# Kernel optimization log

Measured on AMD Instinct MI355X. Metric: run time of the kernel, lower is better.

Reference implementation:

```python
import jax, jax.numpy as jnp
import numpy as np

B, T, V, E, DH, H, M, W = 64, 50, 32000, 64, 128, 8, 256, 50


def setup_inputs() -> dict:
    key = jax.random.key(0)
    ks = jax.random.split(key, 18)
    sc = 0.02
    return {
        "x": jax.random.randint(ks[0], (B, T), 0, V),
        "tok_emb": jax.random.normal(ks[1], (V, E)) * sc,
        "pos_emb": jax.random.normal(ks[2], (W, E)) * sc,
        "Wq": jax.random.normal(ks[3], (H, E, DH)) * sc,
        "bq": jnp.zeros((H, DH)),
        "Wk": jax.random.normal(ks[4], (H, E, DH)) * sc,
        "bk": jnp.zeros((H, DH)),
        "Wv": jax.random.normal(ks[5], (H, E, DH)) * sc,
        "bv": jnp.zeros((H, DH)),
        "Wo": jax.random.normal(ks[6], (H * DH, E)) * sc,
        "bo": jnp.zeros((E,)),
        "W1": jax.random.normal(ks[7], (E, M)) * sc,
        "b1": jnp.zeros((M,)),
        "W2": jax.random.normal(ks[8], (M, E)) * sc,
        "b2": jnp.zeros((E,)),
        "Wf": jax.random.normal(ks[9], (E, V)) * sc,
        "bf": jnp.zeros((V,)),
    }


def reference(x, tok_emb, pos_emb, Wq, bq, Wk, bk, Wv, bv, Wo, bo, W1, b1, W2, b2, Wf, bf):
    b, t = x.shape
    h = tok_emb[x] + pos_emb[:t]  # [B,T,E]
    # batched per-head QKV projections (original loops over 8 heads)
    Q = jnp.einsum("bte,hed->bhtd", h, Wq) + bq[None, :, None, :]
    K = jnp.einsum("bte,hed->bhtd", h, Wk) + bk[None, :, None, :]
    Vv = jnp.einsum("bte,hed->bhtd", h, Wv) + bv[None, :, None, :]
    scores = jnp.einsum("bhtd,bhsd->bhts", Q, K) / (DH ** 0.5)
    # faithful to original: masked_fill(tril(scores) == 0, -inf)
    scores = jnp.where(jnp.tril(scores) == 0, -jnp.inf, scores)
    attn = jax.nn.softmax(scores, axis=-1)
    o = jnp.einsum("bhts,bhsd->bhtd", attn, Vv)
    o = o.transpose(0, 2, 1, 3).reshape(b, t, H * DH)  # concat heads
    a = o @ Wo + bo
    # NOTE: no residual connections in the original module
    m = jax.nn.gelu(a @ W1 + b1, approximate=False)
    y = m @ W2 + b2
    logits = y @ Wf + bf  # [B,T,V]
    return logits
```

## Files before the change

### kernel.cpp

```cpp
#include <hip/hip_runtime.h>
#include <math.h>

#define T_ 50
#define R_ 3200

using u16 = unsigned short;
typedef __attribute__((ext_vector_type(8))) __bf16 bf16x8;
typedef __attribute__((ext_vector_type(4))) float f32x4;

__device__ __forceinline__ float bf2f(u16 u) {
  union { unsigned int i; float f; } x; x.i = ((unsigned int)u) << 16; return x.f;
}
__device__ __forceinline__ u16 f2bf(float f) {
  union { float f; unsigned int i; } x; x.f = f;
  unsigned int r = x.i + 0x7FFFu + ((x.i >> 16) & 1u);
  return (u16)(r >> 16);
}
__device__ __forceinline__ void split2(float v, u16& hi, u16& lo) {
  hi = f2bf(v);
  lo = f2bf(v - bf2f(hi));
}
__device__ __forceinline__ float gelu_f(float v) {
  return 0.5f * v * (1.0f + erff(v * 0.70710678118654752f));
}

__global__ __launch_bounds__(256) void k_embed(const int* __restrict__ x,
    const float* __restrict__ tok, const float* __restrict__ pos,
    float* __restrict__ h) {
  int i = blockIdx.x * 256 + threadIdx.x;
  if (i >= R_ * 64) return;
  int row = i >> 6, e = i & 63;
  int t = row % T_;
  int v = x[row];
  h[i] = tok[(long)v * 64 + e] + pos[t * 64 + e];
}

__global__ __launch_bounds__(256) void k_pack(
    const float* __restrict__ Wq, const float* __restrict__ Wk, const float* __restrict__ Wv,
    const float* __restrict__ bq, const float* __restrict__ bk, const float* __restrict__ bv,
    const float* __restrict__ Wo, const float* __restrict__ W1, const float* __restrict__ W2,
    u16* __restrict__ WqkvTh, u16* __restrict__ WqkvTl, float* __restrict__ bqkv,
    u16* __restrict__ WoTh, u16* __restrict__ WoTl,
    u16* __restrict__ W1Th, u16* __restrict__ W1Tl,
    u16* __restrict__ W2Th, u16* __restrict__ W2Tl) {
  int i = blockIdx.x * 256 + threadIdx.x;
  const int S0 = 196608, S1 = 3072, S2 = 65536, S3 = 16384;
  if (i < S0) {
    int n = i >> 6, e = i & 63;
    int p = n >> 10, rem = n & 1023;
    int hh = rem >> 7, d = rem & 127;
    const float* W = (p == 0) ? Wq : ((p == 1) ? Wk : Wv);
    split2(W[hh * 8192 + e * 128 + d], WqkvTh[i], WqkvTl[i]);
    return;
  }
  i -= S0;
  if (i < S1) { int p = i >> 10, rem = i & 1023;
    const float* bb = (p == 0) ? bq : ((p == 1) ? bk : bv);
    bqkv[i] = bb[rem]; return; }
  i -= S1;
  if (i < S2) { int n = i >> 10, k = i & 1023;
    split2(Wo[k * 64 + n], WoTh[i], WoTl[i]); return; }
  i -= S2;
  if (i < S3) { int n = i >> 6, k = i & 63;
    split2(W1[k * 256 + n], W1Th[i], W1Tl[i]); return; }
  i -= S3;
  { int n = i >> 8, k = i & 255;
    split2(W2[k * 64 + n], W2Th[i], W2Tl[i]); }
}

__global__ __launch_bounds__(256) void k_transpose_wf(const float* __restrict__ Wf,
    u16* __restrict__ WfTh, u16* __restrict__ WfTl) {
  __shared__ __align__(16) float tile[64][68];
  int n0 = blockIdx.x * 64;
  for (int c = threadIdx.x; c < 1024; c += 256) {
    int k = c >> 4, ch = (c & 15) * 4;
    *(float4*)&tile[k][ch] = *(const float4*)&Wf[(long)k * 32000 + n0 + ch];
  }
  __syncthreads();
  for (int c = threadIdx.x; c < 1024; c += 256) {
    int n = c >> 4, ch = (c & 15) * 4;
    u16 th[4], tl[4];
#pragma unroll
    for (int j = 0; j < 4; ++j) split2(tile[ch + j][n], th[j], tl[j]);
    *(ushort4*)&WfTh[(long)(n0 + n) * 64 + ch] = *(ushort4*)th;
    *(ushort4*)&WfTl[(long)(n0 + n) * 64 + ch] = *(ushort4*)tl;
  }
}

__global__ __launch_bounds__(256) void k_attn(const float* __restrict__ QKV,
                                              float* __restrict__ O) {
  int bh = blockIdx.x;
  int b = bh >> 3, hd = bh & 7;
  __shared__ __align__(16) float Kl[T_][128];
  __shared__ __align__(16) float Vl[T_][128];
  const int tid = threadIdx.x, lane = tid & 63, wave = tid >> 6;
  const float* base = QKV + (long)b * T_ * 3072 + hd * 128;
  for (int c = tid; c < T_ * 32; c += 256) {
    int s = c >> 5, c4 = (c & 31) * 4;
    *(float4*)&Kl[s][c4] = *(const float4*)&base[(long)s * 3072 + 1024 + c4];
    *(float4*)&Vl[s][c4] = *(const float4*)&base[(long)s * 3072 + 2048 + c4];
  }
  __syncthreads();
  const float scale = 0.0883883476483184406f;
  for (int r = wave; r < T_; r += 4) {
    float q0 = base[(long)r * 3072 + lane];
    float q1 = base[(long)r * 3072 + 64 + lane];
    float sc = -INFINITY;
    for (int s = 0; s <= r; ++s) {
      float p = q0 * Kl[s][lane] + q1 * Kl[s][64 + lane];
      p += __shfl_xor(p, 32); p += __shfl_xor(p, 16); p += __shfl_xor(p, 8);
      p += __shfl_xor(p, 4);  p += __shfl_xor(p, 2);  p += __shfl_xor(p, 1);
      if (lane == s) sc = p * scale;
    }
    float mx = sc;
    mx = fmaxf(mx, __shfl_xor(mx, 32)); mx = fmaxf(mx, __shfl_xor(mx, 16));
    mx = fmaxf(mx, __shfl_xor(mx, 8));  mx = fmaxf(mx, __shfl_xor(mx, 4));
    mx = fmaxf(mx, __shfl_xor(mx, 2));  mx = fmaxf(mx, __shfl_xor(mx, 1));
    float e = expf(sc - mx);
    float sum = e;
    sum += __shfl_xor(sum, 32); sum += __shfl_xor(sum, 16); sum += __shfl_xor(sum, 8);
    sum += __shfl_xor(sum, 4);  sum += __shfl_xor(sum, 2);  sum += __shfl_xor(sum, 1);
    float pr = e / sum;
    float o0 = 0.f, o1 = 0.f;
    for (int s = 0; s <= r; ++s) {
      float p = __shfl(pr, s);
      o0 += p * Vl[s][lane];
      o1 += p * Vl[s][64 + lane];
    }
    long orow = ((long)b * T_ + r) * 1024 + hd * 128;
    O[orow + lane] = o0;
    O[orow + 64 + lane] = o1;
  }
}

template <int BN, int ACT>
__global__ __launch_bounds__(256) void k_gemm(
    const float* __restrict__ A, int lda,
    const u16* __restrict__ Bth, const u16* __restrict__ Btl,
    const float* __restrict__ bias, float* __restrict__ C, int ldc, int K) {
  constexpr int BM = 64, BK = 64;
  constexpr int TN = BN / 16;
  __shared__ __align__(16) u16 Ah[BM][BK + 8];
  __shared__ __align__(16) u16 Al[BM][BK + 8];
  __shared__ __align__(16) u16 Bh[BN][BK + 8];
  __shared__ __align__(16) u16 Bl[BN][BK + 8];
  const int m0 = blockIdx.x * BM;
  const int n0 = blockIdx.y * BN;
  const int tid = threadIdx.x;
  const int lane = tid & 63, wave = tid >> 6;
  const int ln = lane & 15, quad = lane >> 4;
  const int wm = wave * 16;
  f32x4 acc[TN];
#pragma unroll
  for (int tn = 0; tn < TN; ++tn)
#pragma unroll
    for (int i = 0; i < 4; ++i) acc[tn][i] = 0.f;

  for (int kk = 0; kk < K; kk += BK) {
    for (int c = tid; c < BM * 16; c += 256) {
      int r = c >> 4, c4 = (c & 15) * 4;
      float4 v = *(const float4*)&A[(long)(m0 + r) * lda + kk + c4];
      u16 th[4], tl[4];
      split2(v.x, th[0], tl[0]); split2(v.y, th[1], tl[1]);
      split2(v.z, th[2], tl[2]); split2(v.w, th[3], tl[3]);
      *(ushort4*)&Ah[r][c4] = *(ushort4*)th;
      *(ushort4*)&Al[r][c4] = *(ushort4*)tl;
    }
    for (int c = tid; c < BN * 8; c += 256) {
      int r = c >> 3, c8 = (c & 7) * 8;
      *(uint4*)&Bh[r][c8] = *(const uint4*)&Bth[(long)(n0 + r) * K + kk + c8];
      *(uint4*)&Bl[r][c8] = *(const uint4*)&Btl[(long)(n0 + r) * K + kk + c8];
    }
    __syncthreads();
#pragma unroll
    for (int ks = 0; ks < BK / 32; ++ks) {
      bf16x8 ah = *(const bf16x8*)&Ah[wm + ln][ks * 32 + quad * 8];
      bf16x8 al = *(const bf16x8*)&Al[wm + ln][ks * 32 + quad * 8];
#pragma unroll
      for (int tn = 0; tn < TN; ++tn) {
        bf16x8 bh = *(const bf16x8*)&Bh[tn * 16 + ln][ks * 32 + quad * 8];
        bf16x8 bl = *(const bf16x8*)&Bl[tn * 16 + ln][ks * 32 + quad * 8];
        acc[tn] = __builtin_amdgcn_mfma_f32_16x16x32_bf16(ah, bh, acc[tn], 0, 0, 0);
        acc[tn] = __builtin_amdgcn_mfma_f32_16x16x32_bf16(al, bh, acc[tn], 0, 0, 0);
        acc[tn] = __builtin_amdgcn_mfma_f32_16x16x32_bf16(ah, bl, acc[tn], 0, 0, 0);
      }
    }
    __syncthreads();
  }
#pragma unroll
  for (int tn = 0; tn < TN; ++tn) {
    int col = n0 + tn * 16 + ln;
    float bv = bias[col];
#pragma unroll
    for (int r = 0; r < 4; ++r) {
      float v = acc[tn][r] + bv;
      if (ACT) v = gelu_f(v);
      C[(long)(m0 + wm + quad * 4 + r) * ldc + col] = v;
    }
  }
}

extern "C" void kernel_launch(void* const* d_in, const int* in_sizes, int n_in,
                              void* d_out, int out_size, void* d_ws, size_t ws_size,
                              hipStream_t stream) {
  const int*   x   = (const int*)d_in[0];
  const float* tok = (const float*)d_in[1];
  const float* pos = (const float*)d_in[2];
  const float* Wq  = (const float*)d_in[3];
  const float* bq  = (const float*)d_in[4];
  const float* Wk  = (const float*)d_in[5];
  const float* bk  = (const float*)d_in[6];
  const float* Wv  = (const float*)d_in[7];
  const float* bv  = (const float*)d_in[8];
  const float* Wo  = (const float*)d_in[9];
  const float* bo  = (const float*)d_in[10];
  const float* W1  = (const float*)d_in[11];
  const float* b1  = (const float*)d_in[12];
  const float* W2  = (const float*)d_in[13];
  const float* b2  = (const float*)d_in[14];
  const float* Wf  = (const float*)d_in[15];
  const float* bfv = (const float*)d_in[16];

  char* ws = (char*)d_ws;
  float* h      = (float*)(ws + 0);
  float* QKV    = (float*)(ws + 819200);
  float* o      = (float*)(ws + 40140800);
  float* a      = (float*)(ws + 53248000);
  float* m      = (float*)(ws + 54067200);
  float* y      = (float*)(ws + 57344000);
  u16*  WqkvTh  = (u16*)(ws + 58163200);
  u16*  WqkvTl  = (u16*)(ws + 58556416);
  float* bqkv   = (float*)(ws + 58949632);
  u16*  WoTh    = (u16*)(ws + 58961920);
  u16*  WoTl    = (u16*)(ws + 59092992);
  u16*  W1Th    = (u16*)(ws + 59224064);
  u16*  W1Tl    = (u16*)(ws + 59256832);
  u16*  W2Th    = (u16*)(ws + 59289600);
  u16*  W2Tl    = (u16*)(ws + 59322368);
  u16*  WfTh    = (u16*)(ws + 59355136);
  u16*  WfTl    = (u16*)(ws + 63451136);
  float* out    = (float*)d_out;

  k_embed<<<dim3(800), 256, 0, stream>>>(x, tok, pos, h);
  k_pack<<<dim3(1164), 256, 0, stream>>>(Wq, Wk, Wv, bq, bk, bv, Wo, W1, W2,
      WqkvTh, WqkvTl, bqkv, WoTh, WoTl, W1Th, W1Tl, W2Th, W2Tl);
  k_transpose_wf<<<dim3(500), 256, 0, stream>>>(Wf, WfTh, WfTl);
  k_gemm<128, 0><<<dim3(50, 24), 256, 0, stream>>>(h, 64, WqkvTh, WqkvTl, bqkv, QKV, 3072, 64);
  k_attn<<<dim3(512), 256, 0, stream>>>(QKV, o);
  k_gemm<64, 0><<<dim3(50, 1), 256, 0, stream>>>(o, 1024, WoTh, WoTl, bo, a, 64, 1024);
  k_gemm<128, 1><<<dim3(50, 2), 256, 0, stream>>>(a, 64, W1Th, W1Tl, b1, m, 256, 64);
  k_gemm<64, 0><<<dim3(50, 1), 256, 0, stream>>>(m, 256, W2Th, W2Tl, b2, y, 64, 256);
  k_gemm<128, 0><<<dim3(50, 250), 256, 0, stream>>>(y, 64, WfTh, WfTl, bfv, out, 32000, 64);
}
```

Measured before the change: 736.6 us.

## Fuse prep kernels, pre-split activations to bf16 hi/lo, restructure attention

Merges the embed, weight-pack and Wf-transpose kernels into one launch. Producers now emit activations already split into bf16 hi/lo pairs, so the GEMMs read their A operands straight from global memory instead of converting through shared memory. The Wo and W2 GEMMs use a larger K tile. Attention switches from per-key wave reductions to one key per lane through a padded K tile in LDS. This cuts launches and per-tile conversion work, at the cost of uncoalesced direct A-fragment loads and extra LDS traffic.

```diff
diff --git a/kernel.cpp b/kernel.cpp
--- a/kernel.cpp
+++ b/kernel.cpp
@@ -24,54 +24,55 @@
   return 0.5f * v * (1.0f + erff(v * 0.70710678118654752f));
 }
 
-__global__ __launch_bounds__(256) void k_embed(const int* __restrict__ x,
-    const float* __restrict__ tok, const float* __restrict__ pos,
-    float* __restrict__ h) {
-  int i = blockIdx.x * 256 + threadIdx.x;
-  if (i >= R_ * 64) return;
-  int row = i >> 6, e = i & 63;
-  int t = row % T_;
-  int v = x[row];
-  h[i] = tok[(long)v * 64 + e] + pos[t * 64 + e];
-}
-
-__global__ __launch_bounds__(256) void k_pack(
+__global__ __launch_bounds__(256) void k_prep(
+    const int* __restrict__ x, const float* __restrict__ tok, const float* __restrict__ pos,
     const float* __restrict__ Wq, const float* __restrict__ Wk, const float* __restrict__ Wv,
     const float* __restrict__ bq, const float* __restrict__ bk, const float* __restrict__ bv,
     const float* __restrict__ Wo, const float* __restrict__ W1, const float* __restrict__ W2,
+    const float* __restrict__ Wf,
+    u16* __restrict__ hH, u16* __restrict__ hL,
     u16* __restrict__ WqkvTh, u16* __restrict__ WqkvTl, float* __restrict__ bqkv,
     u16* __restrict__ WoTh, u16* __restrict__ WoTl,
     u16* __restrict__ W1Th, u16* __restrict__ W1Tl,
-    u16* __restrict__ W2Th, u16* __restrict__ W2Tl) {
-  int i = blockIdx.x * 256 + threadIdx.x;
-  const int S0 = 196608, S1 = 3072, S2 = 65536, S3 = 16384;
-  if (i < S0) {
-    int n = i >> 6, e = i & 63;
-    int p = n >> 10, rem = n & 1023;
-    int hh = rem >> 7, d = rem & 127;
-    const float* W = (p == 0) ? Wq : ((p == 1) ? Wk : Wv);
-    split2(W[hh * 8192 + e * 128 + d], WqkvTh[i], WqkvTl[i]);
-    return;
-  }
-  i -= S0;
-  if (i < S1) { int p = i >> 10, rem = i & 1023;
-    const float* bb = (p == 0) ? bq : ((p == 1) ? bk : bv);
-    bqkv[i] = bb[rem]; return; }
-  i -= S1;
-  if (i < S2) { int n = i >> 10, k = i & 1023;
-    split2(Wo[k * 64 + n], WoTh[i], WoTl[i]); return; }
-  i -= S2;
-  if (i < S3) { int n = i >> 6, k = i & 63;
-    split2(W1[k * 256 + n], W1Th[i], W1Tl[i]); return; }
-  i -= S3;
-  { int n = i >> 8, k = i & 255;
-    split2(W2[k * 64 + n], W2Th[i], W2Tl[i]); }
-}
-
-__global__ __launch_bounds__(256) void k_transpose_wf(const float* __restrict__ Wf,
+    u16* __restrict__ W2Th, u16* __restrict__ W2Tl,
     u16* __restrict__ WfTh, u16* __restrict__ WfTl) {
   __shared__ __align__(16) float tile[64][68];
-  int n0 = blockIdx.x * 64;
+  int bid = blockIdx.x;
+  if (bid < 800) {
+    int i = bid * 256 + threadIdx.x;
+    int row = i >> 6, e = i & 63;
+    int t = row % T_;
+    int v = x[row];
+    split2(tok[(long)v * 64 + e] + pos[t * 64 + e], hH[i], hL[i]);
+    return;
+  }
+  if (bid < 1964) {
+    int i = (bid - 800) * 256 + threadIdx.x;
+    const int S0 = 196608, S1 = 3072, S2 = 65536, S3 = 16384;
+    if (i < S0) {
+      int n = i >> 6, e = i & 63;
+      int p = n >> 10, rem = n & 1023;
+      int hh_ = rem >> 7, d = rem & 127;
+      const float* W = (p == 0) ? Wq : ((p == 1) ? Wk : Wv);
+      split2(W[hh_ * 8192 + e * 128 + d], WqkvTh[i], WqkvTl[i]);
+      return;
+    }
+    i -= S0;
+    if (i < S1) { int p = i >> 10, rem = i & 1023;
+      const float* bb = (p == 0) ? bq : ((p == 1) ? bk : bv);
+      bqkv[i] = bb[rem]; return; }
+    i -= S1;
+    if (i < S2) { int n = i >> 10, k = i & 1023;
+      split2(Wo[k * 64 + n], WoTh[i], WoTl[i]); return; }
+    i -= S2;
+    if (i < S3) { int n = i >> 6, k = i & 63;
+      split2(W1[k * 256 + n], W1Th[i], W1Tl[i]); return; }
+    i -= S3;
+    { int n = i >> 8, k = i & 255;
+      split2(W2[k * 64 + n], W2Th[i], W2Tl[i]); }
+    return;
+  }
+  int n0 = (bid - 1964) * 64;
   for (int c = threadIdx.x; c < 1024; c += 256) {
     int k = c >> 4, ch = (c & 15) * 4;
     *(float4*)&tile[k][ch] = *(const float4*)&Wf[(long)k * 32000 + n0 + ch];
@@ -88,30 +89,35 @@
 }
 
 __global__ __launch_bounds__(256) void k_attn(const float* __restrict__ QKV,
-                                              float* __restrict__ O) {
+                                              u16* __restrict__ Oh,
+                                              u16* __restrict__ Ol) {
   int bh = blockIdx.x;
   int b = bh >> 3, hd = bh & 7;
-  __shared__ __align__(16) float Kl[T_][128];
+  __shared__ __align__(16) float Kl[64][133];
   __shared__ __align__(16) float Vl[T_][128];
+  __shared__ float Qw[4][128];
+  __shared__ float Pw[4][64];
   const int tid = threadIdx.x, lane = tid & 63, wave = tid >> 6;
   const float* base = QKV + (long)b * T_ * 3072 + hd * 128;
   for (int c = tid; c < T_ * 32; c += 256) {
     int s = c >> 5, c4 = (c & 31) * 4;
-    *(float4*)&Kl[s][c4] = *(const float4*)&base[(long)s * 3072 + 1024 + c4];
+    float4 kv = *(const float4*)&base[(long)s * 3072 + 1024 + c4];
+    Kl[s][c4] = kv.x; Kl[s][c4 + 1] = kv.y; Kl[s][c4 + 2] = kv.z; Kl[s][c4 + 3] = kv.w;
     *(float4*)&Vl[s][c4] = *(const float4*)&base[(long)s * 3072 + 2048 + c4];
+  }
+  for (int c = tid; c < 14 * 32; c += 256) {
+    int s = 50 + (c >> 5), c4 = (c & 31) * 4;
+    Kl[s][c4] = 0.f; Kl[s][c4 + 1] = 0.f; Kl[s][c4 + 2] = 0.f; Kl[s][c4 + 3] = 0.f;
   }
   __syncthreads();
   const float scale = 0.0883883476483184406f;
   for (int r = wave; r < T_; r += 4) {
-    float q0 = base[(long)r * 3072 + lane];
-    float q1 = base[(long)r * 3072 + 64 + lane];
-    float sc = -INFINITY;
-    for (int s = 0; s <= r; ++s) {
-      float p = q0 * Kl[s][lane] + q1 * Kl[s][64 + lane];
-      p += __shfl_xor(p, 32); p += __shfl_xor(p, 16); p += __shfl_xor(p, 8);
-      p += __shfl_xor(p, 4);  p += __shfl_xor(p, 2);  p += __shfl_xor(p, 1);
-      if (lane == s) sc = p * scale;
-    }
+    Qw[wave][lane] = base[(long)r * 3072 + lane];
+    Qw[wave][64 + lane] = base[(long)r * 3072 + 64 + lane];
+    float p = 0.f;
+#pragma unroll 8
+    for (int d = 0; d < 128; ++d) p += Qw[wave][d] * Kl[lane][d];
+    float sc = (lane <= r) ? p * scale : -INFINITY;
     float mx = sc;
     mx = fmaxf(mx, __shfl_xor(mx, 32)); mx = fmaxf(mx, __shfl_xor(mx, 16));
     mx = fmaxf(mx, __shfl_xor(mx, 8));  mx = fmaxf(mx, __shfl_xor(mx, 4));
@@ -120,36 +126,37 @@
     float sum = e;
     sum += __shfl_xor(sum, 32); sum += __shfl_xor(sum, 16); sum += __shfl_xor(sum, 8);
     sum += __shfl_xor(sum, 4);  sum += __shfl_xor(sum, 2);  sum += __shfl_xor(sum, 1);
-    float pr = e / sum;
+    Pw[wave][lane] = e / sum;
     float o0 = 0.f, o1 = 0.f;
+#pragma unroll 4
     for (int s = 0; s <= r; ++s) {
-      float p = __shfl(pr, s);
-      o0 += p * Vl[s][lane];
-      o1 += p * Vl[s][64 + lane];
+      float pv = Pw[wave][s];
+      o0 += pv * Vl[s][lane];
+      o1 += pv * Vl[s][64 + lane];
     }
     long orow = ((long)b * T_ + r) * 1024 + hd * 128;
-    O[orow + lane] = o0;
-    O[orow + 64 + lane] = o1;
-  }
-}
-
-template <int BN, int ACT>
+    u16 hi, lo;
+    split2(o0, hi, lo); Oh[orow + lane] = hi;      Ol[orow + lane] = lo;
+    split2(o1, hi, lo); Oh[orow + 64 + lane] = hi; Ol[orow + 64 + lane] = lo;
+  }
+}
+
+template <int BN, int BK, int ACT, int OSPLIT>
 __global__ __launch_bounds__(256) void k_gemm(
-    const float* __restrict__ A, int lda,
+    const u16* __restrict__ Ah, const u16* __restrict__ Al,
     const u16* __restrict__ Bth, const u16* __restrict__ Btl,
-    const float* __restrict__ bias, float* __restrict__ C, int ldc, int K) {
-  constexpr int BM = 64, BK = 64;
+    const float* __restrict__ bias,
+    float* __restrict__ C, u16* __restrict__ Ch, u16* __restrict__ Cl,
+    int ldc, int K) {
+  constexpr int BM = 64;
   constexpr int TN = BN / 16;
-  __shared__ __align__(16) u16 Ah[BM][BK + 8];
-  __shared__ __align__(16) u16 Al[BM][BK + 8];
+  constexpr int BKW = BK / 8;
   __shared__ __align__(16) u16 Bh[BN][BK + 8];
   __shared__ __align__(16) u16 Bl[BN][BK + 8];
-  const int m0 = blockIdx.x * BM;
-  const int n0 = blockIdx.y * BN;
-  const int tid = threadIdx.x;
-  const int lane = tid & 63, wave = tid >> 6;
+  const int m0 = blockIdx.x * BM, n0 = blockIdx.y * BN;
+  const int tid = threadIdx.x, lane = tid & 63, wave = tid >> 6;
   const int ln = lane & 15, quad = lane >> 4;
-  const int wm = wave * 16;
+  const long arow = (long)(m0 + wave * 16 + ln) * K;
   f32x4 acc[TN];
 #pragma unroll
   for (int tn = 0; tn < TN; ++tn)
@@ -157,32 +164,25 @@
     for (int i = 0; i < 4; ++i) acc[tn][i] = 0.f;
 
   for (int kk = 0; kk < K; kk += BK) {
-    for (int c = tid; c < BM * 16; c += 256) {
-      int r = c >> 4, c4 = (c & 15) * 4;
-      float4 v = *(const float4*)&A[(long)(m0 + r) * lda + kk + c4];
-      u16 th[4], tl[4];
-      split2(v.x, th[0], tl[0]); split2(v.y, th[1], tl[1]);
-      split2(v.z, th[2], tl[2]); split2(v.w, th[3], tl[3]);
-      *(ushort4*)&Ah[r][c4] = *(ushort4*)th;
-      *(ushort4*)&Al[r][c4] = *(ushort4*)tl;
-    }
-    for (int c = tid; c < BN * 8; c += 256) {
-      int r = c >> 3, c8 = (c & 7) * 8;
+#pragma unroll
+    for (int c0 = 0; c0 < BN * BKW; c0 += 256) {
+      int c = c0 + tid;
+      int r = c / BKW, c8 = (c % BKW) * 8;
       *(uint4*)&Bh[r][c8] = *(const uint4*)&Bth[(long)(n0 + r) * K + kk + c8];
       *(uint4*)&Bl[r][c8] = *(const uint4*)&Btl[(long)(n0 + r) * K + kk + c8];
     }
     __syncthreads();
 #pragma unroll
     for (int ks = 0; ks < BK / 32; ++ks) {
-      bf16x8 ah = *(const bf16x8*)&Ah[wm + ln][ks * 32 + quad * 8];
-      bf16x8 al = *(const bf16x8*)&Al[wm + ln][ks * 32 + quad * 8];
+      bf16x8 a_h = *(const bf16x8*)&Ah[arow + kk + ks * 32 + quad * 8];
+      bf16x8 a_l = *(const bf16x8*)&Al[arow + kk + ks * 32 + quad * 8];
 #pragma unroll
       for (int tn = 0; tn < TN; ++tn) {
-        bf16x8 bh = *(const bf16x8*)&Bh[tn * 16 + ln][ks * 32 + quad * 8];
-        bf16x8 bl = *(const bf16x8*)&Bl[tn * 16 + ln][ks * 32 + quad * 8];
-        acc[tn] = __builtin_amdgcn_mfma_f32_16x16x32_bf16(ah, bh, acc[tn], 0, 0, 0);
-        acc[tn] = __builtin_amdgcn_mfma_f32_16x16x32_bf16(al, bh, acc[tn], 0, 0, 0);
-        acc[tn] = __builtin_amdgcn_mfma_f32_16x16x32_bf16(ah, bl, acc[tn], 0, 0, 0);
+        bf16x8 b_h = *(const bf16x8*)&Bh[tn * 16 + ln][ks * 32 + quad * 8];
+        bf16x8 b_l = *(const bf16x8*)&Bl[tn * 16 + ln][ks * 32 + quad * 8];
+        acc[tn] = __builtin_amdgcn_mfma_f32_16x16x32_bf16(a_h, b_h, acc[tn], 0, 0, 0);
+        acc[tn] = __builtin_amdgcn_mfma_f32_16x16x32_bf16(a_l, b_h, acc[tn], 0, 0, 0);
+        acc[tn] = __builtin_amdgcn_mfma_f32_16x16x32_bf16(a_h, b_l, acc[tn], 0, 0, 0);
       }
     }
     __syncthreads();
@@ -192,10 +192,16 @@
     int col = n0 + tn * 16 + ln;
     float bv = bias[col];
 #pragma unroll
-    for (int r = 0; r < 4; ++r) {
-      float v = acc[tn][r] + bv;
+    for (int rr = 0; rr < 4; ++rr) {
+      float v = acc[tn][rr] + bv;
       if (ACT) v = gelu_f(v);
-      C[(long)(m0 + wm + quad * 4 + r) * ldc + col] = v;
+      long idx = (long)(m0 + wave * 16 + quad * 4 + rr) * ldc + col;
+      if constexpr (OSPLIT) {
+        u16 hi, lo; split2(v, hi, lo);
+        Ch[idx] = hi; Cl[idx] = lo;
+      } else {
+        C[idx] = v;
+      }
     }
   }
 }
@@ -222,33 +228,42 @@
   const float* bfv = (const float*)d_in[16];
 
   char* ws = (char*)d_ws;
-  float* h      = (float*)(ws + 0);
+  u16*   hH     = (u16*)(ws + 0);
+  u16*   hL     = (u16*)(ws + 409600);
   float* QKV    = (float*)(ws + 819200);
-  float* o      = (float*)(ws + 40140800);
-  float* a      = (float*)(ws + 53248000);
-  float* m      = (float*)(ws + 54067200);
-  float* y      = (float*)(ws + 57344000);
-  u16*  WqkvTh  = (u16*)(ws + 58163200);
-  u16*  WqkvTl  = (u16*)(ws + 58556416);
+  u16*   oH     = (u16*)(ws + 40140800);
+  u16*   oL     = (u16*)(ws + 46694400);
+  u16*   aH     = (u16*)(ws + 53248000);
+  u16*   aL     = (u16*)(ws + 53657600);
+  u16*   mH     = (u16*)(ws + 54067200);
+  u16*   mL     = (u16*)(ws + 55705600);
+  u16*   yH     = (u16*)(ws + 57344000);
+  u16*   yL     = (u16*)(ws + 57753600);
+  u16*   WqkvTh = (u16*)(ws + 58163200);
+  u16*   WqkvTl = (u16*)(ws + 58556416);
   float* bqkv   = (float*)(ws + 58949632);
-  u16*  WoTh    = (u16*)(ws + 58961920);
-  u16*  WoTl    = (u16*)(ws + 59092992);
-  u16*  W1Th    = (u16*)(ws + 59224064);
-  u16*  W1Tl    = (u16*)(ws + 59256832);
-  u16*  W2Th    = (u16*)(ws + 59289600);
-  u16*  W2Tl    = (u16*)(ws + 59322368);
-  u16*  WfTh    = (u16*)(ws + 59355136);
-  u16*  WfTl    = (u16*)(ws + 63451136);
+  u16*   WoTh   = (u16*)(ws + 58961920);
+  u16*   WoTl   = (u16*)(ws + 59092992);
+  u16*   W1Th   = (u16*)(ws + 59224064);
+  u16*   W1Tl   = (u16*)(ws + 59256832);
+  u16*   W2Th   = (u16*)(ws + 59289600);
+  u16*   W2Tl   = (u16*)(ws + 59322368);
+  u16*   WfTh   = (u16*)(ws + 59355136);
+  u16*   WfTl   = (u16*)(ws + 63451136);
   float* out    = (float*)d_out;
 
-  k_embed<<<dim3(800), 256, 0, stream>>>(x, tok, pos, h);
-  k_pack<<<dim3(1164), 256, 0, stream>>>(Wq, Wk, Wv, bq, bk, bv, Wo, W1, W2,
-      WqkvTh, WqkvTl, bqkv, WoTh, WoTl, W1Th, W1Tl, W2Th, W2Tl);
-  k_transpose_wf<<<dim3(500), 256, 0, stream>>>(Wf, WfTh, WfTl);
-  k_gemm<128, 0><<<dim3(50, 24), 256, 0, stream>>>(h, 64, WqkvTh, WqkvTl, bqkv, QKV, 3072, 64);
-  k_attn<<<dim3(512), 256, 0, stream>>>(QKV, o);
-  k_gemm<64, 0><<<dim3(50, 1), 256, 0, stream>>>(o, 1024, WoTh, WoTl, bo, a, 64, 1024);
-  k_gemm<128, 1><<<dim3(50, 2), 256, 0, stream>>>(a, 64, W1Th, W1Tl, b1, m, 256, 64);
-  k_gemm<64, 0><<<dim3(50, 1), 256, 0, stream>>>(m, 256, W2Th, W2Tl, b2, y, 64, 256);
-  k_gemm<128, 0><<<dim3(50, 250), 256, 0, stream>>>(y, 64, WfTh, WfTl, bfv, out, 32000, 64);
-}
+  k_prep<<<dim3(2464), 256, 0, stream>>>(x, tok, pos, Wq, Wk, Wv, bq, bk, bv,
+      Wo, W1, W2, Wf, hH, hL, WqkvTh, WqkvTl, bqkv, WoTh, WoTl,
+      W1Th, W1Tl, W2Th, W2Tl, WfTh, WfTl);
+  k_gemm<128, 64, 0, 0><<<dim3(50, 24), 256, 0, stream>>>(
+      hH, hL, WqkvTh, WqkvTl, bqkv, QKV, nullptr, nullptr, 3072, 64);
+  k_attn<<<dim3(512), 256, 0, stream>>>(QKV, oH, oL);
+  k_gemm<64, 256, 0, 1><<<dim3(50, 1), 256, 0, stream>>>(
+      oH, oL, WoTh, WoTl, bo, nullptr, aH, aL, 64, 1024);
+  k_gemm<128, 64, 1, 1><<<dim3(50, 2), 256, 0, stream>>>(
+      aH, aL, W1Th, W1Tl, b1, nullptr, mH, mL, 256, 64);
+  k_gemm<64, 256, 0, 1><<<dim3(50, 1), 256, 0, stream>>>(
+      mH, mL, W2Th, W2Tl, b2, nullptr, yH, yL, 64, 256);
+  k_gemm<128, 64, 0, 0><<<dim3(50, 250), 256, 0, stream>>>(
+      yH, yL, WfTh, WfTl, bfv, out, nullptr, nullptr, 32000, 64);
+}
```

After: 602.8 us. 18.2% less time.
